# Kernel tuning notes

Hardware: AMD Instinct MI355X
Metric: run time of the kernel (lower is better)

Reference implementation:

```python
import jax, jax.numpy as jnp
import numpy as np

NO_EDGE_OFFSET_T_NORM = 2.0    # pushes no_edge above data range so min() ignores it
NO_EDGE_OFFSET_T_CONORM = -1.0 # pushes no_edge below data range so max() ignores it


def _daa_layer(x, sel, is_t_norm):
    """One DAALayer with a single operator for all nodes (LAYER_WISE init).

    x:   [B, in_features] float
    sel: [out_features, in_features] int, edge type per (node, input):
         0 = no_edge (value 0 + operator-dependent offset), 1 = normal_edge (value x)
    """
    off = NO_EDGE_OFFSET_T_NORM if is_t_norm else NO_EDGE_OFFSET_T_CONORM
    # [B, out, in]: gather edge values per node according to hard routing
    vals = jnp.where(sel[None, :, :] == 1, x[:, None, :], jnp.float32(off))
    # t-norm 'min' / t-conorm 'max' reduction over incoming edges
    return vals.min(axis=-1) if is_t_norm else vals.max(axis=-1)


def setup_inputs() -> dict:
    key = jax.random.key(0)
    k1, k2, k3 = jax.random.split(key, 3)
    B, IN, HID = 256, 1024, 512
    x = jax.random.uniform(k1, (B, IN), dtype=jnp.float32)
    # hard gumbel-softmax over all-ones logits == uniform edge-type choice
    sel0 = jax.random.randint(k2, (HID, IN), 0, 2)  # layer 0: 1024 -> 512
    sel1 = jax.random.randint(k3, (IN, HID), 0, 2)  # layer 1: 512 -> 1024
    return {"x": x, "sel0": sel0, "sel1": sel1}


def reference(x, sel0, sel1):
    h = _daa_layer(x, sel0, True)    # layer 0: T_Norm.min on all nodes
    out = _daa_layer(h, sel1, False)  # layer 1: T_Conorm.max on all nodes
    return out
```

## Files before the change

kernel.cpp:

```cpp
#include <hip/hip_runtime.h>
#include <hip/hip_fp16.h>


#define H_PINF 0x7C00u
#define H_NINF 0xFC00u

__device__ __forceinline__ unsigned pk_add(unsigned a, unsigned b) {
    unsigned r; asm("v_pk_add_f16 %0, %1, %2" : "=v"(r) : "v"(a), "v"(b)); return r;
}
__device__ __forceinline__ unsigned pk_min(unsigned a, unsigned b) {
    unsigned r; asm("v_pk_min_f16 %0, %1, %2" : "=v"(r) : "v"(a), "v"(b)); return r;
}
__device__ __forceinline__ unsigned pk_max(unsigned a, unsigned b) {
    unsigned r; asm("v_pk_max_f16 %0, %1, %2" : "=v"(r) : "v"(a), "v"(b)); return r;
}
__device__ __forceinline__ unsigned hpk(float a, float b) {
    return (unsigned)__half_as_ushort(__float2half(a))
         | ((unsigned)__half_as_ushort(__float2half(b)) << 16);
}
__device__ __forceinline__ float h2f(unsigned short u) {
    __half h = *reinterpret_cast<__half*>(&u);
    return __half2float(h);
}
__device__ __forceinline__ unsigned selpk(int a, int b, unsigned inf) {
    return (a ? 0u : inf) | ((b ? 0u : inf) << 16);
}

__global__ __launch_bounds__(1024) void daa_l0(
    const float* __restrict__ x, const int* __restrict__ sel0,
    uint4* __restrict__ hS)
{
    __shared__ unsigned aW[8 * 512];
    __shared__ uint4 xL[2][16 * 65];
    __shared__ unsigned short red[16 * 8 * 64];
    __shared__ unsigned short mrg[8 * 64];

    const int tid  = threadIdx.x;
    const int lane = tid & 63;
    const int s    = __builtin_amdgcn_readfirstlane(tid >> 6);
    const int bch  = blockIdx.x & 3;
    const int j    = blockIdx.x >> 2;
    const int b0   = bch * 64;

    {
        const int4* sp = (const int4*)sel0;
        const int row = tid >> 7, ch = tid & 127;
        const int4 v0 = sp[(size_t)(8 * j + row) * 256 + ch * 2 + 0];
        const int4 v1 = sp[(size_t)(8 * j + row) * 256 + ch * 2 + 1];
        unsigned* dst = &aW[row * 512 + ch * 4];
        dst[0] = selpk(v0.x, v0.y, H_PINF);
        dst[1] = selpk(v0.z, v0.w, H_PINF);
        dst[2] = selpk(v1.x, v1.y, H_PINF);
        dst[3] = selpk(v1.z, v1.w, H_PINF);
    }

    const int br = tid >> 4, cg = tid & 15;
#define STAGE(T, BUF)                                                      \
    do {                                                                   \
        const float* xr = x + (size_t)(b0 + br) * 1024 + (T) * 128 + cg * 8; \
        const float4 f0 = ((const float4*)xr)[0];                          \
        const float4 f1 = ((const float4*)xr)[1];                          \
        uint4 w;                                                           \
        w.x = hpk(f0.x, f0.y);  w.y = hpk(f0.z, f0.w);                     \
        w.z = hpk(f1.x, f1.y);  w.w = hpk(f1.z, f1.w);                     \
        xL[BUF][cg * 65 + br] = w;                                         \
    } while (0)

    STAGE(0, 0);
    __syncthreads();

    unsigned acc[8];
#pragma unroll
    for (int r = 0; r < 8; ++r) acc[r] = hpk(2.0f, 2.0f);

#pragma unroll
    for (int t = 0; t < 8; ++t) {
        if (t + 1 < 8) STAGE(t + 1, (t + 1) & 1);
        const uint4 xv = xL[t & 1][s * 65 + lane];
#pragma unroll
        for (int r = 0; r < 8; ++r) {
            const unsigned* a = &aW[r * 512 + t * 64 + s * 4];
            acc[r] = pk_min(acc[r], pk_add(xv.x, a[0]));
            acc[r] = pk_min(acc[r], pk_add(xv.y, a[1]));
            acc[r] = pk_min(acc[r], pk_add(xv.z, a[2]));
            acc[r] = pk_min(acc[r], pk_add(xv.w, a[3]));
        }
        __syncthreads();
    }
#undef STAGE

    {
#pragma unroll
        for (int r = 0; r < 8; ++r) {
            const unsigned f = pk_min(acc[r], acc[r] >> 16);
            red[(s * 8 + r) * 64 + lane] = (unsigned short)(f & 0xffffu);
        }
    }
    __syncthreads();

    if (tid < 512) {
        const int u = tid >> 6, ln = tid & 63;
        unsigned m = red[u * 64 + ln];
#pragma unroll
        for (int ss = 1; ss < 16; ++ss)
            m = pk_min(m, (unsigned)red[(ss * 8 + u) * 64 + ln]);
        mrg[u * 64 + ln] = (unsigned short)(m & 0xffffu);
    }
    __syncthreads();

    if (tid < 64) {
        uint4 w;
        w.x = (unsigned)mrg[0 * 64 + tid] | ((unsigned)mrg[1 * 64 + tid] << 16);
        w.y = (unsigned)mrg[2 * 64 + tid] | ((unsigned)mrg[3 * 64 + tid] << 16);
        w.z = (unsigned)mrg[4 * 64 + tid] | ((unsigned)mrg[5 * 64 + tid] << 16);
        w.w = (unsigned)mrg[6 * 64 + tid] | ((unsigned)mrg[7 * 64 + tid] << 16);
        hS[(size_t)bch * 4096 + (size_t)j * 64 + tid] = w;
    }
}

__global__ __launch_bounds__(1024) void daa_l1(
    const uint4* __restrict__ hS, const int* __restrict__ sel1,
    float* __restrict__ out)
{
    __shared__ unsigned aW[16 * 256];
    __shared__ unsigned short red[16 * 16 * 64];
    __shared__ float redf[16 * 65];

    const int tid  = threadIdx.x;
    const int lane = tid & 63;
    const int s    = __builtin_amdgcn_readfirstlane(tid >> 6);
    const int bch  = blockIdx.x & 3;
    const int j2   = blockIdx.x >> 2;
    const int b0   = bch * 64;

    {
        const int4* sp = (const int4*)sel1;
        const int row = tid >> 6, ch = tid & 63;
        const int4 v0 = sp[(size_t)(16 * j2 + row) * 128 + ch * 2 + 0];
        const int4 v1 = sp[(size_t)(16 * j2 + row) * 128 + ch * 2 + 1];
        unsigned* dst = &aW[row * 256 + ch * 4];
        dst[0] = selpk(v0.x, v0.y, H_NINF);
        dst[1] = selpk(v0.z, v0.w, H_NINF);
        dst[2] = selpk(v1.x, v1.y, H_NINF);
        dst[3] = selpk(v1.z, v1.w, H_NINF);
    }

    uint4 xh[4];
#pragma unroll
    for (int k = 0; k < 4; ++k)
        xh[k] = hS[(size_t)bch * 4096 + (size_t)(s * 4 + k) * 64 + lane];

    __syncthreads();

    unsigned acc[16];
#pragma unroll
    for (int r = 0; r < 16; ++r) acc[r] = hpk(-1.0f, -1.0f);

#pragma unroll
    for (int r = 0; r < 16; ++r) {
        const unsigned* a = &aW[r * 256 + s * 16];
#pragma unroll
        for (int k = 0; k < 4; ++k) {
            acc[r] = pk_max(acc[r], pk_add(xh[k].x, a[k * 4 + 0]));
            acc[r] = pk_max(acc[r], pk_add(xh[k].y, a[k * 4 + 1]));
            acc[r] = pk_max(acc[r], pk_add(xh[k].z, a[k * 4 + 2]));
            acc[r] = pk_max(acc[r], pk_add(xh[k].w, a[k * 4 + 3]));
        }
    }

    {
#pragma unroll
        for (int r = 0; r < 16; ++r) {
            const unsigned f = pk_max(acc[r], acc[r] >> 16);
            red[(s * 16 + r) * 64 + lane] = (unsigned short)(f & 0xffffu);
        }
    }
    __syncthreads();

    {
        const int u = tid >> 6, ln = tid & 63;
        unsigned m = red[u * 64 + ln];
#pragma unroll
        for (int ss = 1; ss < 16; ++ss)
            m = pk_max(m, (unsigned)red[(ss * 16 + u) * 64 + ln]);
        redf[u * 65 + ln] = h2f((unsigned short)(m & 0xffffu));
    }
    __syncthreads();

    {
        const int b = tid >> 4, ol = tid & 15;
        out[(size_t)(b0 + b) * 1024 + 16 * j2 + ol] = redf[ol * 65 + b];
    }
}

extern "C" void kernel_launch(void* const* d_in, const int* in_sizes, int n_in,
                              void* d_out, int out_size, void* d_ws, size_t ws_size,
                              hipStream_t stream) {
    const float* x    = (const float*)d_in[0];
    const int*   sel0 = (const int*)d_in[1];
    const int*   sel1 = (const int*)d_in[2];
    float* out = (float*)d_out;

    uint4* hS = (uint4*)d_ws;

    daa_l0<<<256, 1024, 0, stream>>>(x, sel0, hS);
    daa_l1<<<256, 1024, 0, stream>>>(hS, sel1, out);
}
```

Baseline: 21.62 us.

## Prepack half of selection rows to global and read them via uniform loads

```diff
diff --git a/kernel.cpp b/kernel.cpp
--- a/kernel.cpp
+++ b/kernel.cpp
@@ -26,14 +26,37 @@
     return (a ? 0u : inf) | ((b ? 0u : inf) << 16);
 }
 
+__global__ __launch_bounds__(256) void pack_sc(
+    const int* __restrict__ sel0, const int* __restrict__ sel1,
+    unsigned* __restrict__ a0h, unsigned* __restrict__ a1h)
+{
+    const int t = blockIdx.x * 256 + threadIdx.x;
+    {
+        const int jr = t >> 8, i4 = t & 255;
+        const int srow = (jr >> 2) * 8 + 4 + (jr & 3);
+        const int4 v = ((const int4*)sel0)[(size_t)srow * 256 + i4];
+        unsigned* d = &a0h[(size_t)jr * 512 + i4 * 2];
+        d[0] = selpk(v.x, v.y, H_PINF);
+        d[1] = selpk(v.z, v.w, H_PINF);
+    }
+    {
+        const int jr = t >> 7, i4 = t & 127;
+        const int srow = (jr >> 3) * 16 + 8 + (jr & 7);
+        const int4 v = ((const int4*)sel1)[(size_t)srow * 128 + i4];
+        unsigned* d = &a1h[(size_t)jr * 256 + i4 * 2];
+        d[0] = selpk(v.x, v.y, H_NINF);
+        d[1] = selpk(v.z, v.w, H_NINF);
+    }
+}
+
 __global__ __launch_bounds__(1024) void daa_l0(
     const float* __restrict__ x, const int* __restrict__ sel0,
-    uint4* __restrict__ hS)
+    const unsigned* __restrict__ a0h, uint4* __restrict__ hS)
 {
-    __shared__ unsigned aW[8 * 512];
-    __shared__ uint4 xL[2][16 * 65];
-    __shared__ unsigned short red[16 * 8 * 64];
-    __shared__ unsigned short mrg[8 * 64];
+    __shared__ unsigned aW[4 * 512];
+    __shared__ uint4 xL[2][32 * 65];
+    __shared__ unsigned red32[16 * 4 * 64];
+    __shared__ unsigned mrg32[4 * 64];
 
     const int tid  = threadIdx.x;
     const int lane = tid & 63;
@@ -43,27 +66,28 @@
     const int b0   = bch * 64;
 
     {
-        const int4* sp = (const int4*)sel0;
-        const int row = tid >> 7, ch = tid & 127;
-        const int4 v0 = sp[(size_t)(8 * j + row) * 256 + ch * 2 + 0];
-        const int4 v1 = sp[(size_t)(8 * j + row) * 256 + ch * 2 + 1];
-        unsigned* dst = &aW[row * 512 + ch * 4];
-        dst[0] = selpk(v0.x, v0.y, H_PINF);
-        dst[1] = selpk(v0.z, v0.w, H_PINF);
-        dst[2] = selpk(v1.x, v1.y, H_PINF);
-        dst[3] = selpk(v1.z, v1.w, H_PINF);
+        const int row = tid >> 8, ch = tid & 255;
+        const int4 v = ((const int4*)sel0)[(size_t)(8 * j + row) * 256 + ch];
+        unsigned* d = &aW[row * 512 + ch * 2];
+        d[0] = selpk(v.x, v.y, H_PINF);
+        d[1] = selpk(v.z, v.w, H_PINF);
     }
 
     const int br = tid >> 4, cg = tid & 15;
-#define STAGE(T, BUF)                                                      \
-    do {                                                                   \
-        const float* xr = x + (size_t)(b0 + br) * 1024 + (T) * 128 + cg * 8; \
-        const float4 f0 = ((const float4*)xr)[0];                          \
-        const float4 f1 = ((const float4*)xr)[1];                          \
-        uint4 w;                                                           \
-        w.x = hpk(f0.x, f0.y);  w.y = hpk(f0.z, f0.w);                     \
-        w.z = hpk(f1.x, f1.y);  w.w = hpk(f1.z, f1.w);                     \
-        xL[BUF][cg * 65 + br] = w;                                         \
+#define STAGE(T, BUF)                                                        \
+    do {                                                                     \
+        const float* xr = x + (size_t)(b0 + br) * 1024 + (T) * 256 + cg * 16; \
+        const float4 f0 = ((const float4*)xr)[0];                            \
+        const float4 f1 = ((const float4*)xr)[1];                            \
+        const float4 f2 = ((const float4*)xr)[2];                            \
+        const float4 f3 = ((const float4*)xr)[3];                            \
+        uint4 w0, w1;                                                        \
+        w0.x = hpk(f0.x, f0.y);  w0.y = hpk(f0.z, f0.w);                     \
+        w0.z = hpk(f1.x, f1.y);  w0.w = hpk(f1.z, f1.w);                     \
+        w1.x = hpk(f2.x, f2.y);  w1.y = hpk(f2.z, f2.w);                     \
+        w1.z = hpk(f3.x, f3.y);  w1.w = hpk(f3.z, f3.w);                     \
+        xL[BUF][(cg * 2 + 0) * 65 + br] = w0;                                \
+        xL[BUF][(cg * 2 + 1) * 65 + br] = w1;                                \
     } while (0)
 
     STAGE(0, 0);
@@ -74,16 +98,33 @@
     for (int r = 0; r < 8; ++r) acc[r] = hpk(2.0f, 2.0f);
 
 #pragma unroll
-    for (int t = 0; t < 8; ++t) {
-        if (t + 1 < 8) STAGE(t + 1, (t + 1) & 1);
-        const uint4 xv = xL[t & 1][s * 65 + lane];
-#pragma unroll
-        for (int r = 0; r < 8; ++r) {
-            const unsigned* a = &aW[r * 512 + t * 64 + s * 4];
-            acc[r] = pk_min(acc[r], pk_add(xv.x, a[0]));
-            acc[r] = pk_min(acc[r], pk_add(xv.y, a[1]));
-            acc[r] = pk_min(acc[r], pk_add(xv.z, a[2]));
-            acc[r] = pk_min(acc[r], pk_add(xv.w, a[3]));
+    for (int t = 0; t < 4; ++t) {
+        if (t + 1 < 4) STAGE(t + 1, (t + 1) & 1);
+        const uint4 xv0 = xL[t & 1][(2 * s + 0) * 65 + lane];
+        const uint4 xv1 = xL[t & 1][(2 * s + 1) * 65 + lane];
+#pragma unroll
+        for (int r = 0; r < 4; ++r) {
+            const unsigned* a = &aW[r * 512 + t * 128 + s * 8];
+            acc[r] = pk_min(acc[r], pk_add(xv0.x, a[0]));
+            acc[r] = pk_min(acc[r], pk_add(xv0.y, a[1]));
+            acc[r] = pk_min(acc[r], pk_add(xv0.z, a[2]));
+            acc[r] = pk_min(acc[r], pk_add(xv0.w, a[3]));
+            acc[r] = pk_min(acc[r], pk_add(xv1.x, a[4]));
+            acc[r] = pk_min(acc[r], pk_add(xv1.y, a[5]));
+            acc[r] = pk_min(acc[r], pk_add(xv1.z, a[6]));
+            acc[r] = pk_min(acc[r], pk_add(xv1.w, a[7]));
+        }
+#pragma unroll
+        for (int r = 0; r < 4; ++r) {
+            const unsigned* a = &a0h[(size_t)(j * 4 + r) * 512 + t * 128 + s * 8];
+            acc[4 + r] = pk_min(acc[4 + r], pk_add(xv0.x, a[0]));
+            acc[4 + r] = pk_min(acc[4 + r], pk_add(xv0.y, a[1]));
+            acc[4 + r] = pk_min(acc[4 + r], pk_add(xv0.z, a[2]));
+            acc[4 + r] = pk_min(acc[4 + r], pk_add(xv0.w, a[3]));
+            acc[4 + r] = pk_min(acc[4 + r], pk_add(xv1.x, a[4]));
+            acc[4 + r] = pk_min(acc[4 + r], pk_add(xv1.y, a[5]));
+            acc[4 + r] = pk_min(acc[4 + r], pk_add(xv1.z, a[6]));
+            acc[4 + r] = pk_min(acc[4 + r], pk_add(xv1.w, a[7]));
         }
         __syncthreads();
     }
@@ -91,39 +132,40 @@
 
     {
 #pragma unroll
-        for (int r = 0; r < 8; ++r) {
-            const unsigned f = pk_min(acc[r], acc[r] >> 16);
-            red[(s * 8 + r) * 64 + lane] = (unsigned short)(f & 0xffffu);
-        }
-    }
-    __syncthreads();
-
-    if (tid < 512) {
+        for (int u = 0; u < 4; ++u) {
+            const unsigned flo = pk_min(acc[2 * u + 0], acc[2 * u + 0] >> 16);
+            const unsigned fhi = pk_min(acc[2 * u + 1], acc[2 * u + 1] >> 16);
+            red32[(s * 4 + u) * 64 + lane] = (flo & 0xffffu) | (fhi << 16);
+        }
+    }
+    __syncthreads();
+
+    if (tid < 256) {
         const int u = tid >> 6, ln = tid & 63;
-        unsigned m = red[u * 64 + ln];
+        unsigned m = red32[u * 64 + ln];
 #pragma unroll
         for (int ss = 1; ss < 16; ++ss)
-            m = pk_min(m, (unsigned)red[(ss * 8 + u) * 64 + ln]);
-        mrg[u * 64 + ln] = (unsigned short)(m & 0xffffu);
+            m = pk_min(m, red32[(ss * 4 + u) * 64 + ln]);
+        mrg32[u * 64 + ln] = m;
     }
     __syncthreads();
 
     if (tid < 64) {
         uint4 w;
-        w.x = (unsigned)mrg[0 * 64 + tid] | ((unsigned)mrg[1 * 64 + tid] << 16);
-        w.y = (unsigned)mrg[2 * 64 + tid] | ((unsigned)mrg[3 * 64 + tid] << 16);
-        w.z = (unsigned)mrg[4 * 64 + tid] | ((unsigned)mrg[5 * 64 + tid] << 16);
-        w.w = (unsigned)mrg[6 * 64 + tid] | ((unsigned)mrg[7 * 64 + tid] << 16);
+        w.x = mrg32[0 * 64 + tid];
+        w.y = mrg32[1 * 64 + tid];
+        w.z = mrg32[2 * 64 + tid];
+        w.w = mrg32[3 * 64 + tid];
         hS[(size_t)bch * 4096 + (size_t)j * 64 + tid] = w;
     }
 }
 
 __global__ __launch_bounds__(1024) void daa_l1(
     const uint4* __restrict__ hS, const int* __restrict__ sel1,
-    float* __restrict__ out)
+    const unsigned* __restrict__ a1h, float* __restrict__ out)
 {
-    __shared__ unsigned aW[16 * 256];
-    __shared__ unsigned short red[16 * 16 * 64];
+    __shared__ unsigned aW[8 * 256];
+    __shared__ unsigned red32[16 * 8 * 64];
     __shared__ float redf[16 * 65];
 
     const int tid  = threadIdx.x;
@@ -134,15 +176,11 @@
     const int b0   = bch * 64;
 
     {
-        const int4* sp = (const int4*)sel1;
-        const int row = tid >> 6, ch = tid & 63;
-        const int4 v0 = sp[(size_t)(16 * j2 + row) * 128 + ch * 2 + 0];
-        const int4 v1 = sp[(size_t)(16 * j2 + row) * 128 + ch * 2 + 1];
-        unsigned* dst = &aW[row * 256 + ch * 4];
-        dst[0] = selpk(v0.x, v0.y, H_NINF);
-        dst[1] = selpk(v0.z, v0.w, H_NINF);
-        dst[2] = selpk(v1.x, v1.y, H_NINF);
-        dst[3] = selpk(v1.z, v1.w, H_NINF);
+        const int row = tid >> 7, ch = tid & 127;
+        const int4 v = ((const int4*)sel1)[(size_t)(16 * j2 + row) * 128 + ch];
+        unsigned* d = &aW[row * 256 + ch * 2];
+        d[0] = selpk(v.x, v.y, H_NINF);
+        d[1] = selpk(v.z, v.w, H_NINF);
     }
 
     uint4 xh[4];
@@ -157,7 +195,7 @@
     for (int r = 0; r < 16; ++r) acc[r] = hpk(-1.0f, -1.0f);
 
 #pragma unroll
-    for (int r = 0; r < 16; ++r) {
+    for (int r = 0; r < 8; ++r) {
         const unsigned* a = &aW[r * 256 + s * 16];
 #pragma unroll
         for (int k = 0; k < 4; ++k) {
@@ -167,23 +205,36 @@
             acc[r] = pk_max(acc[r], pk_add(xh[k].w, a[k * 4 + 3]));
         }
     }
-
-    {
-#pragma unroll
-        for (int r = 0; r < 16; ++r) {
-            const unsigned f = pk_max(acc[r], acc[r] >> 16);
-            red[(s * 16 + r) * 64 + lane] = (unsigned short)(f & 0xffffu);
-        }
-    }
-    __syncthreads();
-
-    {
+#pragma unroll
+    for (int r = 0; r < 8; ++r) {
+        const unsigned* a = &a1h[(size_t)(j2 * 8 + r) * 256 + s * 16];
+#pragma unroll
+        for (int k = 0; k < 4; ++k) {
+            acc[8 + r] = pk_max(acc[8 + r], pk_add(xh[k].x, a[k * 4 + 0]));
+            acc[8 + r] = pk_max(acc[8 + r], pk_add(xh[k].y, a[k * 4 + 1]));
+            acc[8 + r] = pk_max(acc[8 + r], pk_add(xh[k].z, a[k * 4 + 2]));
+            acc[8 + r] = pk_max(acc[8 + r], pk_add(xh[k].w, a[k * 4 + 3]));
+        }
+    }
+
+    {
+#pragma unroll
+        for (int u = 0; u < 8; ++u) {
+            const unsigned flo = pk_max(acc[2 * u + 0], acc[2 * u + 0] >> 16);
+            const unsigned fhi = pk_max(acc[2 * u + 1], acc[2 * u + 1] >> 16);
+            red32[(s * 8 + u) * 64 + lane] = (flo & 0xffffu) | (fhi << 16);
+        }
+    }
+    __syncthreads();
+
+    if (tid < 512) {
         const int u = tid >> 6, ln = tid & 63;
-        unsigned m = red[u * 64 + ln];
+        unsigned m = red32[u * 64 + ln];
 #pragma unroll
         for (int ss = 1; ss < 16; ++ss)
-            m = pk_max(m, (unsigned)red[(ss * 16 + u) * 64 + ln]);
-        redf[u * 65 + ln] = h2f((unsigned short)(m & 0xffffu));
+            m = pk_max(m, red32[(ss * 8 + u) * 64 + ln]);
+        redf[(2 * u + 0) * 65 + ln] = h2f((unsigned short)(m & 0xffffu));
+        redf[(2 * u + 1) * 65 + ln] = h2f((unsigned short)(m >> 16));
     }
     __syncthreads();
 
@@ -201,8 +252,12 @@
     const int*   sel1 = (const int*)d_in[2];
     float* out = (float*)d_out;
 
-    uint4* hS = (uint4*)d_ws;
-
-    daa_l0<<<256, 1024, 0, stream>>>(x, sel0, hS);
-    daa_l1<<<256, 1024, 0, stream>>>(hS, sel1, out);
-}
+    char* ws = (char*)d_ws;
+    uint4*    hS  = (uint4*)ws;
+    unsigned* a0h = (unsigned*)(ws + (256 << 10));
+    unsigned* a1h = (unsigned*)(ws + (768 << 10));
+
+    pack_sc<<<256, 256, 0, stream>>>(sel0, sel1, a0h, a1h);
+    daa_l0<<<256, 1024, 0, stream>>>(x, sel0, a0h, hS);
+    daa_l1<<<256, 1024, 0, stream>>>(hS, sel1, a1h, out);
+}
```

Measured after the change: 29.14 us. 1.35x slower.
